# Kernel optimization log

Hardware: AMD Instinct MI355X
Metric: run time of the kernel (lower is better)

The kernel has to match this reference:

```python
import jax, jax.numpy as jnp
import numpy as np

EPS = 1e-4
# 8 box corners as min/max selection bits (matches the torch cat order:
# mmm, mmx, mxm, mxx, xmm, xmx, xxm, xxx)
_BITS = jnp.array([[0,0,0],[0,0,1],[0,1,0],[0,1,1],[1,0,0],[1,0,1],[1,1,0],[1,1,1]], dtype=jnp.float32)


def setup_inputs() -> dict:
    key = jax.random.key(0)
    k1, k2, k3, k4, k5 = jax.random.split(key, 5)
    K = 1024
    bb_min = jax.random.uniform(k1, (K, 3), minval=-1.0, maxval=1.0)
    size = jax.random.uniform(k2, (K, 3), minval=0.05, maxval=0.4)
    bb_max = bb_min + size
    # well-conditioned affine transforms: near-identity linear block + translation
    R = jnp.eye(3, dtype=jnp.float32) + 0.1 * jax.random.normal(k3, (K, 3, 3))
    t = 0.5 * jax.random.normal(k4, (K, 3))
    top = jnp.concatenate([R, t[:, :, None]], axis=-1)            # [K,3,4]
    bottom = jnp.broadcast_to(jnp.array([[0.0, 0.0, 0.0, 1.0]], dtype=jnp.float32), (K, 1, 4))
    abs_transforms = jnp.concatenate([top, bottom], axis=1)       # [K,4,4]
    selfpen_disable_mat = jax.random.randint(k5, (K, K), 0, 2) > 0
    return {"bb_min": bb_min, "bb_max": bb_max,
            "abs_transforms": abs_transforms,
            "selfpen_disable_mat": selfpen_disable_mat}


def reference(bb_min, bb_max, abs_transforms, selfpen_disable_mat):
    K = bb_min.shape[0]
    bits = _BITS.astype(bb_min.dtype)
    # corners: [K,8,3]
    corners = bb_min[:, None, :] * (1.0 - bits) + bb_max[:, None, :] * bits
    hcorners = jnp.concatenate([corners, jnp.ones((K, 8, 1), dtype=bb_min.dtype)], axis=-1)  # [K,8,4]
    # pose each box's corners by its own transform
    hposed = jnp.einsum('kij,kcj->kci', abs_transforms, hcorners)  # [K,8,4]
    # project every posed corner into every box's local frame
    back_trans = jnp.linalg.inv(abs_transforms)                    # [K,4,4]
    proj = jnp.einsum('kij,lcj->klci', back_trans, hposed)[..., :3]  # [K,K,8,3]
    inside = ((proj > bb_min[:, None, None, :] + EPS)
              & (proj < bb_max[:, None, None, :] - EPS)).all(axis=-1).any(axis=-1)  # [K,K]
    inside = inside & selfpen_disable_mat
    inside = inside | inside.T
    inside = jnp.tril(inside)
    # fixed-size index extraction (pad with -1): equivalent of
    # torch.stack(torch.where(inside)).sort(dim=0)[0].t()
    rows, cols = jnp.nonzero(inside, size=K * K, fill_value=-1)
    inds = jnp.stack([jnp.minimum(rows, cols), jnp.maximum(rows, cols)], axis=-1)  # [K*K,2], padded with -1
    return hposed[..., :3], inds
```

## Files before the change

kernel.cpp:

```cpp
#include <hip/hip_runtime.h>
#include <stdint.h>

#define KBOX 1024
#define EPSF 1e-4f
#define SLACK 3e-5f
#define TILE_BLOCKS 4096
#define POSE_BLOCKS 4

#define BM_OFF 0
#define TC_OFF 131072

__device__ inline void inv_affine(const float r[12], float* o) {
    double m00 = r[0], m01 = r[1], m02 = r[2];
    double m10 = r[4], m11 = r[5], m12 = r[6];
    double m20 = r[8], m21 = r[9], m22 = r[10];
    double c00 = m11 * m22 - m12 * m21;
    double c01 = m12 * m20 - m10 * m22;
    double c02 = m10 * m21 - m11 * m20;
    double det = m00 * c00 + m01 * c01 + m02 * c02;
    double id = 1.0 / det;
    double i00 = c00 * id, i01 = (m02 * m21 - m01 * m22) * id, i02 = (m01 * m12 - m02 * m11) * id;
    double i10 = c01 * id, i11 = (m00 * m22 - m02 * m20) * id, i12 = (m02 * m10 - m00 * m12) * id;
    double i20 = c02 * id, i21 = (m01 * m20 - m00 * m21) * id, i22 = (m00 * m11 - m01 * m10) * id;
    double tx = r[3], ty = r[7], tz = r[11];
    o[0] = (float)i00; o[1] = (float)i01; o[2] = (float)i02;
    o[3] = (float)(-(i00 * tx + i01 * ty + i02 * tz));
    o[4] = (float)i10; o[5] = (float)i11; o[6] = (float)i12;
    o[7] = (float)(-(i10 * tx + i11 * ty + i12 * tz));
    o[8] = (float)i20; o[9] = (float)i21; o[10] = (float)i22;
    o[11] = (float)(-(i20 * tx + i21 * ty + i22 * tz));
}

__global__ void k_main(const float* __restrict__ bbmin, const float* __restrict__ bbmax,
                       const float* __restrict__ A, const uint8_t* __restrict__ disB,
                       float* __restrict__ out_hposed, float* __restrict__ out_pairs,
                       uint64_t* __restrict__ bm, uint32_t* __restrict__ tileCnt) {
    int bid = blockIdx.x;
    int t = threadIdx.x;

    if (bid >= TILE_BLOCKS) {
        int k = (bid - TILE_BLOCKS) * 256 + t;
        float r[12];
#pragma unroll
        for (int i = 0; i < 3; ++i) {
            float4 a4 = *(const float4*)(A + (size_t)k * 16 + i * 4);
            r[i * 4 + 0] = a4.x; r[i * 4 + 1] = a4.y; r[i * 4 + 2] = a4.z; r[i * 4 + 3] = a4.w;
        }
        float bmn[3], bmx[3];
#pragma unroll
        for (int i = 0; i < 3; ++i) { bmn[i] = bbmin[k * 3 + i]; bmx[i] = bbmax[k * 3 + i]; }
#pragma unroll
        for (int c = 0; c < 8; ++c) {
            float cx = ((c >> 2) & 1) ? bmx[0] : bmn[0];
            float cy = ((c >> 1) & 1) ? bmx[1] : bmn[1];
            float cz = (c & 1) ? bmx[2] : bmn[2];
#pragma unroll
            for (int i = 0; i < 3; ++i)
                out_hposed[(size_t)k * 24 + c * 3 + i] =
                    r[i * 4 + 0] * cx + r[i * 4 + 1] * cy + r[i * 4 + 2] * cz + r[i * 4 + 3];
        }
        return;
    }

    int k = bid >> 2, j = bid & 3;
    int lane = t & 63, wave = t >> 6;

    ((float2*)out_pairs)[(size_t)bid * 256 + t] = make_float2(-1.f, -1.f);

    if (j * 256 > k) {
        if (t < 4) tileCnt[(size_t)k * 4 + j] = 0;
        return;
    }
    int l = j * 256 + t;

    uint32_t dw = ((const uint32_t*)disB)[lane];
    const bool isBool = __ballot((dw & 0xFFFFFF00u) != 0 ? 1 : 0) != 0ull;

    float rk[12];
#pragma unroll
    for (int i = 0; i < 3; ++i) {
        float4 a4 = *(const float4*)(A + (size_t)k * 16 + i * 4);
        rk[i * 4 + 0] = a4.x; rk[i * 4 + 1] = a4.y; rk[i * 4 + 2] = a4.z; rk[i * 4 + 3] = a4.w;
    }
    float bmnk[3], bmxk[3];
#pragma unroll
    for (int i = 0; i < 3; ++i) { bmnk[i] = bbmin[k * 3 + i]; bmxk[i] = bbmax[k * 3 + i]; }
    float wmnk[3], wmxk[3];
    {
        float cx = 0.5f * (bmnk[0] + bmxk[0]), hx = 0.5f * (bmxk[0] - bmnk[0]);
        float cy = 0.5f * (bmnk[1] + bmxk[1]), hy = 0.5f * (bmxk[1] - bmnk[1]);
        float cz = 0.5f * (bmnk[2] + bmxk[2]), hz = 0.5f * (bmxk[2] - bmnk[2]);
#pragma unroll
        for (int i = 0; i < 3; ++i) {
            float c = rk[i * 4 + 0] * cx + rk[i * 4 + 1] * cy + rk[i * 4 + 2] * cz + rk[i * 4 + 3];
            float h = fabsf(rk[i * 4 + 0]) * hx + fabsf(rk[i * 4 + 1]) * hy + fabsf(rk[i * 4 + 2]) * hz;
            wmnk[i] = c - h - SLACK;
            wmxk[i] = c + h + SLACK;
        }
    }

    float rl[12];
#pragma unroll
    for (int i = 0; i < 3; ++i) {
        float4 a4 = *(const float4*)(A + (size_t)l * 16 + i * 4);
        rl[i * 4 + 0] = a4.x; rl[i * 4 + 1] = a4.y; rl[i * 4 + 2] = a4.z; rl[i * 4 + 3] = a4.w;
    }
    float bmnl[3], bmxl[3];
#pragma unroll
    for (int i = 0; i < 3; ++i) { bmnl[i] = bbmin[l * 3 + i]; bmxl[i] = bbmax[l * 3 + i]; }
    float wcl[3], whl[3];
    {
        float cx = 0.5f * (bmnl[0] + bmxl[0]), hx = 0.5f * (bmxl[0] - bmnl[0]);
        float cy = 0.5f * (bmnl[1] + bmxl[1]), hy = 0.5f * (bmxl[1] - bmnl[1]);
        float cz = 0.5f * (bmnl[2] + bmxl[2]), hz = 0.5f * (bmxl[2] - bmnl[2]);
#pragma unroll
        for (int i = 0; i < 3; ++i) {
            wcl[i] = rl[i * 4 + 0] * cx + rl[i * 4 + 1] * cy + rl[i * 4 + 2] * cz + rl[i * 4 + 3];
            whl[i] = fabsf(rl[i * 4 + 0]) * hx + fabsf(rl[i * 4 + 1]) * hy + fabsf(rl[i * 4 + 2]) * hz;
        }
    }

    bool cand = false;
    if (l <= k) {
        cand = (wcl[0] - whl[0] <= wmxk[0]) & (wmnk[0] <= wcl[0] + whl[0]) &
               (wcl[1] - whl[1] <= wmxk[1]) & (wmnk[1] <= wcl[1] + whl[1]) &
               (wcl[2] - whl[2] <= wmxk[2]) & (wmnk[2] <= wcl[2] + whl[2]);
    }
    bool bit = false, dA = false, dB = false;
    if (cand) {
        if (isBool) {
            dA = disB[(size_t)k * KBOX + l] != 0;
            dB = disB[(size_t)l * KBOX + k] != 0;
        } else {
            const int* disI = (const int*)disB;
            dA = disI[(size_t)k * KBOX + l] != 0;
            dB = disI[(size_t)l * KBOX + k] != 0;
        }
    }
    if (cand && (dA | dB)) {
        if (dA) {
            float bk[12];
            inv_affine(rk, bk);
            bool rawA = false;
#pragma unroll
            for (int c = 0; c < 8; ++c) {
                float cx = ((c >> 2) & 1) ? bmxl[0] : bmnl[0];
                float cy = ((c >> 1) & 1) ? bmxl[1] : bmnl[1];
                float cz = (c & 1) ? bmxl[2] : bmnl[2];
                float px = rl[0] * cx + rl[1] * cy + rl[2] * cz + rl[3];
                float py = rl[4] * cx + rl[5] * cy + rl[6] * cz + rl[7];
                float pz = rl[8] * cx + rl[9] * cy + rl[10] * cz + rl[11];
                float x = bk[0] * px + bk[1] * py + bk[2] * pz + bk[3];
                float y = bk[4] * px + bk[5] * py + bk[6] * pz + bk[7];
                float z = bk[8] * px + bk[9] * py + bk[10] * pz + bk[11];
                rawA = rawA || (x > bmnk[0] + EPSF && x < bmxk[0] - EPSF &&
                                y > bmnk[1] + EPSF && y < bmxk[1] - EPSF &&
                                z > bmnk[2] + EPSF && z < bmxk[2] - EPSF);
            }
            bit = rawA;
        }
        if (dB && !bit) {
            float bl[12];
            inv_affine(rl, bl);
            bool rawB = false;
#pragma unroll
            for (int c = 0; c < 8; ++c) {
                float cx = ((c >> 2) & 1) ? bmxk[0] : bmnk[0];
                float cy = ((c >> 1) & 1) ? bmxk[1] : bmnk[1];
                float cz = (c & 1) ? bmxk[2] : bmnk[2];
                float px = rk[0] * cx + rk[1] * cy + rk[2] * cz + rk[3];
                float py = rk[4] * cx + rk[5] * cy + rk[6] * cz + rk[7];
                float pz = rk[8] * cx + rk[9] * cy + rk[10] * cz + rk[11];
                float x = bl[0] * px + bl[1] * py + bl[2] * pz + bl[3];
                float y = bl[4] * px + bl[5] * py + bl[6] * pz + bl[7];
                float z = bl[8] * px + bl[9] * py + bl[10] * pz + bl[11];
                rawB = rawB || (x > bmnl[0] + EPSF && x < bmxl[0] - EPSF &&
                                y > bmnl[1] + EPSF && y < bmxl[1] - EPSF &&
                                z > bmnl[2] + EPSF && z < bmxl[2] - EPSF);
            }
            bit = rawB;
        }
    }
    uint64_t word = __ballot(bit ? 1 : 0);
    __shared__ uint32_t wcnt[4];
    if (lane == 0) {
        bm[(size_t)k * 16 + j * 4 + wave] = word;
        wcnt[wave] = (uint32_t)__popcll(word);
    }
    __syncthreads();
    if (t == 0) tileCnt[(size_t)k * 4 + j] = wcnt[0] + wcnt[1] + wcnt[2] + wcnt[3];
}

__global__ void k_compact(const uint64_t* __restrict__ bm,
                          const uint32_t* __restrict__ tileCnt, float* __restrict__ out) {
    int k = blockIdx.x;
    int t = threadIdx.x;
    int wave = t >> 6, lane = t & 63;
    __shared__ uint32_t ws4[4];
    uint32_t s = 0;
#pragma unroll
    for (int rr = 0; rr < 4; ++rr) {
        int row = t + rr * 256;
        uint4 c4 = *(const uint4*)(tileCnt + (size_t)row * 4);
        uint32_t v = c4.x + c4.y + c4.z + c4.w;
        s += (row < k) ? v : 0u;
    }
#pragma unroll
    for (int off = 32; off > 0; off >>= 1) s += __shfl_xor(s, off);
    if (lane == 0) ws4[wave] = s;
    __syncthreads();
    if (t >= 64) return;
    uint32_t start = ws4[0] + ws4[1] + ws4[2] + ws4[3];

    uint64_t w = (t < 16 && t * 64 <= k) ? bm[(size_t)k * 16 + t] : 0ull;
    int c = (int)__popcll(w);
    int p = c;
#pragma unroll
    for (int off = 1; off < 64; off <<= 1) {
        int u = __shfl_up(p, off);
        if (t >= off) p += u;
    }
    int ofs = (int)start + (p - c);
    float fk = (float)k;
    while (w) {
        int b = __builtin_ctzll(w);
        int col = t * 64 + b;
        out[2 * (size_t)ofs + 0] = (float)col;
        out[2 * (size_t)ofs + 1] = fk;
        ++ofs;
        w &= w - 1;
    }
}

extern "C" void kernel_launch(void* const* d_in, const int* in_sizes, int n_in,
                              void* d_out, int out_size, void* d_ws, size_t ws_size,
                              hipStream_t stream) {
    const float* bbmin = (const float*)d_in[0];
    const float* bbmax = (const float*)d_in[1];
    const float* A = (const float*)d_in[2];
    const uint8_t* dis = (const uint8_t*)d_in[3];
    float* out = (float*)d_out;

    char* ws = (char*)d_ws;
    uint64_t* bm = (uint64_t*)(ws + BM_OFF);
    uint32_t* tileCnt = (uint32_t*)(ws + TC_OFF);

    k_main<<<TILE_BLOCKS + POSE_BLOCKS, 256, 0, stream>>>(
        bbmin, bbmax, A, dis, out, out + KBOX * 24, bm, tileCnt);
    k_compact<<<KBOX, 256, 0, stream>>>(bm, tileCnt, out + KBOX * 24);
}
```

Measured before the change: 21.26 us.

## Launch only lower-triangular tiles and move padding fill into compaction

The main kernel now launches only the active lower-triangular tiles, mapping block ids to (row, tile) pairs piecewise, so it no longer spends blocks on empty upper-triangle tiles. The -1 padding of the pair output moves from the main kernel into the compaction kernel, which now writes only entries past the total count. Compaction processes four rows per block with one wave per row, cutting the block count by four. Inactive tileCnt entries are no longer zeroed and are instead masked out when read.

```diff
diff --git a/kernel.cpp b/kernel.cpp
--- a/kernel.cpp
+++ b/kernel.cpp
@@ -4,7 +4,7 @@
 #define KBOX 1024
 #define EPSF 1e-4f
 #define SLACK 3e-5f
-#define TILE_BLOCKS 4096
+#define ACT_TILES 2560
 #define POSE_BLOCKS 4
 
 #define BM_OFF 0
@@ -33,13 +33,13 @@
 
 __global__ void k_main(const float* __restrict__ bbmin, const float* __restrict__ bbmax,
                        const float* __restrict__ A, const uint8_t* __restrict__ disB,
-                       float* __restrict__ out_hposed, float* __restrict__ out_pairs,
+                       float* __restrict__ out_hposed,
                        uint64_t* __restrict__ bm, uint32_t* __restrict__ tileCnt) {
     int bid = blockIdx.x;
     int t = threadIdx.x;
 
-    if (bid >= TILE_BLOCKS) {
-        int k = (bid - TILE_BLOCKS) * 256 + t;
+    if (bid >= ACT_TILES) {
+        int k = (bid - ACT_TILES) * 256 + t;
         float r[12];
 #pragma unroll
         for (int i = 0; i < 3; ++i) {
@@ -62,15 +62,12 @@
         return;
     }
 
-    int k = bid >> 2, j = bid & 3;
+    int k, j;
+    if (bid < 256)       { k = bid;                      j = 0; }
+    else if (bid < 768)  { k = 256 + ((bid - 256) >> 1); j = (bid - 256) & 1; }
+    else if (bid < 1536) { k = 512 + (bid - 768) / 3;    j = (bid - 768) % 3; }
+    else                 { k = 768 + ((bid - 1536) >> 2);j = (bid - 1536) & 3; }
     int lane = t & 63, wave = t >> 6;
-
-    ((float2*)out_pairs)[(size_t)bid * 256 + t] = make_float2(-1.f, -1.f);
-
-    if (j * 256 > k) {
-        if (t < 4) tileCnt[(size_t)k * 4 + j] = 0;
-        return;
-    }
     int l = j * 256 + t;
 
     uint32_t dw = ((const uint32_t*)disB)[lane];
@@ -193,38 +190,57 @@
 
 __global__ void k_compact(const uint64_t* __restrict__ bm,
                           const uint32_t* __restrict__ tileCnt, float* __restrict__ out) {
-    int k = blockIdx.x;
+    int b = blockIdx.x;
     int t = threadIdx.x;
     int wave = t >> 6, lane = t & 63;
-    __shared__ uint32_t ws4[4];
-    uint32_t s = 0;
+    int k0 = 4 * b;
+    __shared__ uint32_t baseW[4], totW[4], rowc[4];
+
+    uint32_t sm = 0, st = 0;
 #pragma unroll
     for (int rr = 0; rr < 4; ++rr) {
         int row = t + rr * 256;
         uint4 c4 = *(const uint4*)(tileCnt + (size_t)row * 4);
-        uint32_t v = c4.x + c4.y + c4.z + c4.w;
-        s += (row < k) ? v : 0u;
-    }
-#pragma unroll
-    for (int off = 32; off > 0; off >>= 1) s += __shfl_xor(s, off);
-    if (lane == 0) ws4[wave] = s;
+        uint32_t v = c4.x + ((row >= 256) ? c4.y : 0u) + ((row >= 512) ? c4.z : 0u) +
+                     ((row >= 768) ? c4.w : 0u);
+        sm += (row < k0) ? v : 0u;
+        st += v;
+    }
+#pragma unroll
+    for (int off = 32; off > 0; off >>= 1) { sm += __shfl_xor(sm, off); st += __shfl_xor(st, off); }
+    if (lane == 0) { baseW[wave] = sm; totW[wave] = st; }
+    if (t < 4) {
+        int row = k0 + t;
+        uint4 c4 = *(const uint4*)(tileCnt + (size_t)row * 4);
+        rowc[t] = c4.x + ((row >= 256) ? c4.y : 0u) + ((row >= 512) ? c4.z : 0u) +
+                  ((row >= 768) ? c4.w : 0u);
+    }
     __syncthreads();
-    if (t >= 64) return;
-    uint32_t start = ws4[0] + ws4[1] + ws4[2] + ws4[3];
-
-    uint64_t w = (t < 16 && t * 64 <= k) ? bm[(size_t)k * 16 + t] : 0ull;
+    uint32_t base = baseW[0] + baseW[1] + baseW[2] + baseW[3];
+    uint32_t total = totW[0] + totW[1] + totW[2] + totW[3];
+
+    float2* o2 = (float2*)out;
+    for (uint32_t i = total + (uint32_t)b * 256 + t; i < (uint32_t)(KBOX * KBOX); i += 256 * 256)
+        o2[i] = make_float2(-1.f, -1.f);
+
+    uint32_t startw = base;
+#pragma unroll
+    for (int r = 0; r < 4; ++r)
+        if (r < wave) startw += rowc[r];
+    int k = k0 + wave;
+    uint64_t w = (lane < 16 && lane * 64 <= k) ? bm[(size_t)k * 16 + lane] : 0ull;
     int c = (int)__popcll(w);
     int p = c;
 #pragma unroll
     for (int off = 1; off < 64; off <<= 1) {
         int u = __shfl_up(p, off);
-        if (t >= off) p += u;
-    }
-    int ofs = (int)start + (p - c);
+        if (lane >= off) p += u;
+    }
+    int ofs = (int)startw + (p - c);
     float fk = (float)k;
     while (w) {
-        int b = __builtin_ctzll(w);
-        int col = t * 64 + b;
+        int bpos = __builtin_ctzll(w);
+        int col = lane * 64 + bpos;
         out[2 * (size_t)ofs + 0] = (float)col;
         out[2 * (size_t)ofs + 1] = fk;
         ++ofs;
@@ -245,7 +261,7 @@
     uint64_t* bm = (uint64_t*)(ws + BM_OFF);
     uint32_t* tileCnt = (uint32_t*)(ws + TC_OFF);
 
-    k_main<<<TILE_BLOCKS + POSE_BLOCKS, 256, 0, stream>>>(
-        bbmin, bbmax, A, dis, out, out + KBOX * 24, bm, tileCnt);
-    k_compact<<<KBOX, 256, 0, stream>>>(bm, tileCnt, out + KBOX * 24);
-}
+    k_main<<<ACT_TILES + POSE_BLOCKS, 256, 0, stream>>>(
+        bbmin, bbmax, A, dis, out, bm, tileCnt);
+    k_compact<<<256, 256, 0, stream>>>(bm, tileCnt, out + KBOX * 24);
+}
```

Result: faster. 19.15 us (-9.9%).
